# Optimization experiments

Measured on AMD Instinct MI355X. Metric: run time of the kernel, lower is better.

Reference implementation:

```python
import jax, jax.numpy as jnp
import numpy as np

H = 12  # num_attention_heads


def setup_inputs() -> dict:
    key = jax.random.key(0)
    ks = jax.random.split(key, 7)
    B, T, L, D = 4, 64, 128, 768
    input_ids = jax.random.randint(ks[0], (B, T, L), 0, 30000, dtype=jnp.int32)
    speaker_ids = jax.random.randint(ks[1], (B, T), 0, 8, dtype=jnp.int32)
    token_embeddings = jax.random.normal(ks[2], (B, T, L, D), dtype=jnp.float32)
    edu_embeddings = jax.random.normal(ks[3], (B, T, D), dtype=jnp.float32)
    s = 1.0 / np.sqrt(D)
    Wk = jax.random.normal(ks[4], (D, D), dtype=jnp.float32) * s
    Wv = jax.random.normal(ks[5], (D, D), dtype=jnp.float32) * s
    Wq = jax.random.normal(ks[6], (D, D), dtype=jnp.float32) * s
    return {"input_ids": input_ids, "speaker_ids": speaker_ids,
            "token_embeddings": token_embeddings, "edu_embeddings": edu_embeddings,
            "Wk": Wk, "Wv": Wv, "Wq": Wq}


def reference(input_ids, speaker_ids, token_embeddings, edu_embeddings, Wk, Wv, Wq):
    B, T, L = input_ids.shape
    D = token_embeddings.shape[-1]
    d = D // H
    # per-turn keys/values, split into heads: [B,T,H,d]
    k = (edu_embeddings @ Wk.T).reshape(B, T, H, d)
    v = (edu_embeddings @ Wv.T).reshape(B, T, H, d)
    # per-head outer products k (x) v: [B,T,H,d,d]
    kv = jnp.einsum('bthd,bthe->bthde', k, v)
    # speaker-segmented inclusive prefix sum: M[b,t] = sum_{u<=t, spk[u]==spk[t]} kv[b,u]
    same = speaker_ids[:, None, :] == speaker_ids[:, :, None]        # [B,T(t),T(u)]
    causal = jnp.tril(jnp.ones((T, T), dtype=bool))                  # u <= t (inclusive)
    A = (same & causal).astype(kv.dtype)                             # [B,T,T]
    M = jnp.einsum('btu,buhde->bthde', A, kv)                        # [B,T,H,d,d]
    # token queries attend into their turn's speaker memory matrix
    q = (token_embeddings @ Wq.T).reshape(B, T, L, H, d)
    a = jnp.einsum('btlhd,bthde->btlhe', q, M).reshape(B, T, L, D)
    return token_embeddings + a
```

## Files before the change

### kernel.cpp

```cpp
#include <hip/hip_runtime.h>
#include <hip/hip_bf16.h>

#define NB 4
#define NT 64
#define NL 128
#define ND 768
#define NH 12
#define HD 64

typedef __attribute__((ext_vector_type(8))) short short8;
typedef __attribute__((ext_vector_type(4))) float f32x4;

typedef __attribute__((address_space(3))) unsigned int lds_u32;
typedef __attribute__((address_space(1))) const unsigned int glob_u32;

static __device__ __forceinline__ unsigned short f2b(float x) {
    __hip_bfloat16 h = __float2bfloat16(x);
    return *reinterpret_cast<unsigned short*>(&h);
}
static __device__ __forceinline__ float b2f(unsigned short u) {
    unsigned int v = ((unsigned int)u) << 16;
    union { unsigned int i; float f; } c; c.i = v; return c.f;
}
static __device__ __forceinline__ void gl2lds16(const void* g, void* l) {
    __builtin_amdgcn_global_load_lds((glob_u32*)g, (lds_u32*)l, 16, 0, 0);
}

#define TE_C   3145728u
#define WQ_C   3219456u
#define EDU_C  3244032u
#define WK_C   3317760u
#define NCHUNK 3391488u

__global__ __launch_bounds__(256) void conv_bf16(
    const float* __restrict__ te, const float* __restrict__ Wq,
    const float* __restrict__ edu, const float* __restrict__ Wk,
    const float* __restrict__ Wv, unsigned short* __restrict__ dst)
{
    for (size_t c = (size_t)blockIdx.x * 256 + threadIdx.x; c < (size_t)NCHUNK;
         c += (size_t)2048 * 256) {
        const float* s;
        if (c < TE_C)       s = te  + c * 8;
        else if (c < WQ_C)  s = Wq  + (c - TE_C)  * 8;
        else if (c < EDU_C) s = edu + (c - WQ_C)  * 8;
        else if (c < WK_C)  s = Wk  + (c - EDU_C) * 8;
        else                s = Wv  + (c - WK_C)  * 8;
        float4 x = *(const float4*)s;
        float4 y = *(const float4*)(s + 4);
        unsigned short v[8];
        v[0] = f2b(x.x); v[1] = f2b(x.y); v[2] = f2b(x.z); v[3] = f2b(x.w);
        v[4] = f2b(y.x); v[5] = f2b(y.y); v[6] = f2b(y.z); v[7] = f2b(y.w);
        *(short8*)(dst + c * 8) = *(short8*)v;
    }
}

__global__ __launch_bounds__(256) void kvm(
    const unsigned short* __restrict__ edu_b,
    const unsigned short* __restrict__ wk_b,
    const unsigned short* __restrict__ wv_b,
    const int* __restrict__ spk,
    unsigned short* __restrict__ Mt)
{
    const int h = blockIdx.x, b = blockIdx.y, eh = blockIdx.z;

    __shared__ float bucket[8][32][65];
    __shared__ float k_s[64][68];
    __shared__ float v_s[64][36];
    __shared__ __align__(16) unsigned short stage[10240];
    __shared__ int spk_s[64];
    unsigned short* edu_s = stage;
    unsigned short* wk_s  = stage + 4096;
    unsigned short* wv_s  = stage + 8192;

    const int tid = threadIdx.x, lane = tid & 63, wvx = tid >> 6;
    const int lr = lane & 15, lg = lane >> 4, r8 = lane >> 3, l8 = lane & 7;

    { float* p = &bucket[0][0][0];
      for (int i = tid; i < 8 * 32 * 65; i += 256) p[i] = 0.f; }
    if (tid < 64) spk_s[tid] = spk[b * NT + tid];

    const unsigned short* edub = edu_b + (size_t)(b * 64) * ND;
    const unsigned short* wkb  = wk_b + (size_t)(h * 64) * ND;
    const unsigned short* wvb  = wv_b + (size_t)(h * 64 + eh * 32) * ND;

    f32x4 acc_k[4], acc_v[2];
    #pragma unroll
    for (int i = 0; i < 4; i++) acc_k[i] = (f32x4){0.f, 0.f, 0.f, 0.f};
    #pragma unroll
    for (int i = 0; i < 2; i++) acc_v[i] = (f32x4){0.f, 0.f, 0.f, 0.f};

    const int sswz = ((l8 ^ r8) * 8);

    for (int k0 = 0; k0 < ND; k0 += 64) {
        __syncthreads();
        #pragma unroll
        for (int j = 0; j < 5; j++) {
            const int cid = wvx * 5 + j;
            const unsigned short* gs; unsigned short* ls;
            if (cid < 8)       { gs = edub + (size_t)(cid * 8 + r8) * ND;        ls = edu_s + cid * 512; }
            else if (cid < 16) { gs = wkb  + (size_t)((cid - 8) * 8 + r8) * ND;  ls = wk_s + (cid - 8) * 512; }
            else               { gs = wvb  + (size_t)((cid - 16) * 8 + r8) * ND; ls = wv_s + (cid - 16) * 512; }
            gl2lds16(gs + k0 + sswz, ls);
        }
        __syncthreads();
        #pragma unroll
        for (int k32 = 0; k32 < 2; k32++) {
            const int cx = (((k32 * 4 + lg) ^ (lr & 7)) * 8);
            short8 eb = *(const short8*)&edu_s[(wvx * 16 + lr) * 64 + cx];
            #pragma unroll
            for (int jb = 0; jb < 4; jb++) {
                short8 ak = *(const short8*)&wk_s[(jb * 16 + lr) * 64 + cx];
                acc_k[jb] = __builtin_amdgcn_mfma_f32_16x16x32_bf16(ak, eb, acc_k[jb], 0, 0, 0);
            }
            #pragma unroll
            for (int jb = 0; jb < 2; jb++) {
                short8 av = *(const short8*)&wv_s[(jb * 16 + lr) * 64 + cx];
                acc_v[jb] = __builtin_amdgcn_mfma_f32_16x16x32_bf16(av, eb, acc_v[jb], 0, 0, 0);
            }
        }
    }

    {
        const int t = wvx * 16 + lr;
        #pragma unroll
        for (int jb = 0; jb < 4; jb++) *(f32x4*)&k_s[t][jb * 16 + lg * 4] = acc_k[jb];
        #pragma unroll
        for (int jb = 0; jb < 2; jb++) *(f32x4*)&v_s[t][jb * 16 + lg * 4] = acc_v[jb];
    }
    __syncthreads();

    const int e = tid & 31, dg = tid >> 5;
    for (int t = 0; t < NT; t++) {
        const int s = spk_s[t];
        const float vv = v_s[t][e];
        unsigned short tmp[8];
        #pragma unroll
        for (int jj = 0; jj < 8; jj++) {
            float m = bucket[s][e][dg * 8 + jj] + k_s[t][dg * 8 + jj] * vv;
            bucket[s][e][dg * 8 + jj] = m;
            tmp[jj] = f2b(m);
        }
        unsigned short* mpp = Mt + (((size_t)(b * NT + t) * NH + h) * HD + eh * 32 + e) * HD + dg * 8;
        *(short8*)mpp = *(short8*)tmp;
    }
}

__global__ __launch_bounds__(256, 2) void fused_qm(
    const unsigned short* __restrict__ te_b,
    const unsigned short* __restrict__ wq_b,
    const unsigned short* __restrict__ Mt,
    float* __restrict__ out)
{
    const int orig = blockIdx.x;
    const int id   = (orig & 7) * 192 + (orig >> 3);
    const int hp   = id % 6;
    const int bt   = id / 6;

    __shared__ __align__(16) unsigned short smem[40960];
    unsigned short* mt_s = smem + 32768;
    unsigned short* q_s  = smem;

    const int tid  = threadIdx.x;
    const int lane = tid & 63;
    const int wvx  = tid >> 6;
    const int lr   = lane & 15;
    const int lg   = lane >> 4;
    const int wm   = wvx >> 1;
    const int wn   = wvx & 1;
    const int r8   = lane >> 3;
    const int l8   = lane & 7;
    const int sswz = (l8 ^ r8) * 8;

    const unsigned short* teb = te_b + (size_t)bt * NL * ND;
    const unsigned short* wqb = wq_b + (size_t)hp * 128 * ND;

    {
        const unsigned short* mp = Mt + ((size_t)bt * NH + hp * 2) * (HD * HD);
        #pragma unroll
        for (int j = 0; j < 4; j++) {
            const int off = wvx * 2048 + j * 512;
            gl2lds16(mp + off + r8 * 64 + sswz, mt_s + off);
        }
    }

    f32x4 acc[4][4];
    #pragma unroll
    for (int i = 0; i < 4; i++)
        #pragma unroll
        for (int j = 0; j < 4; j++) acc[i][j] = (f32x4){0.f, 0.f, 0.f, 0.f};

    auto STAGE = [&](int bb, int k0) {
        #pragma unroll
        for (int j = 0; j < 4; j++) {
            const int rbase = wvx * 32 + j * 8;
            gl2lds16(teb + (size_t)(rbase + r8) * ND + k0 + sswz,
                     smem + bb + rbase * 64);
            gl2lds16(wqb + (size_t)(rbase + r8) * ND + k0 + sswz,
                     smem + bb + 8192 + rbase * 64);
        }
    };
    auto COMPUTE = [&](int bb) {
        const unsigned short* tes = smem + bb;
        const unsigned short* wqs = smem + bb + 8192;
        #pragma unroll
        for (int k32 = 0; k32 < 2; k32++) {
            const int cx = (((k32 * 4 + lg) ^ (lr & 7)) * 8);
            short8 af[4], bf[4];
            #pragma unroll
            for (int tm = 0; tm < 4; tm++)
                af[tm] = *(const short8*)&wqs[(wm * 64 + tm * 16 + lr) * 64 + cx];
            #pragma unroll
            for (int tn = 0; tn < 4; tn++)
                bf[tn] = *(const short8*)&tes[(wn * 64 + tn * 16 + lr) * 64 + cx];
            #pragma unroll
            for (int tm = 0; tm < 4; tm++)
                #pragma unroll
                for (int tn = 0; tn < 4; tn++)
                    acc[tm][tn] = __builtin_amdgcn_mfma_f32_16x16x32_bf16(
                        af[tm], bf[tn], acc[tm][tn], 0, 0, 0);
        }
    };

    STAGE(0, 0);
    __syncthreads();
    for (int k0 = 0; k0 < ND; k0 += 128) {
        STAGE(16384, k0 + 64);
        COMPUTE(0);
        __syncthreads();
        if (k0 + 128 < ND) STAGE(0, k0 + 128);
        COMPUTE(16384);
        __syncthreads();
    }

    #pragma unroll
    for (int tm = 0; tm < 4; tm++) {
        const int d0 = wm * 64 + tm * 16 + lg * 4;
        #pragma unroll
        for (int tn = 0; tn < 4; tn++) {
            const int ltok = wn * 64 + tn * 16 + lr;
            f32x4 a = acc[tm][tn];
            uint2 w2;
            w2.x = (unsigned)f2b(a.x) | ((unsigned)f2b(a.y) << 16);
            w2.y = (unsigned)f2b(a.z) | ((unsigned)f2b(a.w) << 16);
            *(uint2*)&q_s[ltok * 136 + d0] = w2;
        }
    }
    __syncthreads();

    const int h2 = wvx & 1;
    const int lh = wvx >> 1;
    f32x4 acc2[4][4];
    #pragma unroll
    for (int i = 0; i < 4; i++)
        #pragma unroll
        for (int j = 0; j < 4; j++) acc2[i][j] = (f32x4){0.f, 0.f, 0.f, 0.f};

    #pragma unroll
    for (int k32 = 0; k32 < 2; k32++) {
        const int ko = k32 * 32 + lg * 8;
        const int cx = (((k32 * 4 + lg) ^ (lr & 7)) * 8);
        short8 af[4], bf[4];
        #pragma unroll
        for (int tm = 0; tm < 4; tm++)
            af[tm] = *(const short8*)&q_s[(lh * 64 + tm * 16 + lr) * 136 + h2 * 64 + ko];
        #pragma unroll
        for (int tn = 0; tn < 4; tn++)
            bf[tn] = *(const short8*)&mt_s[(h2 * 64 + tn * 16 + lr) * 64 + cx];
        #pragma unroll
        for (int tm = 0; tm < 4; tm++)
            #pragma unroll
            for (int tn = 0; tn < 4; tn++)
                acc2[tm][tn] = __builtin_amdgcn_mfma_f32_16x16x32_bf16(
                    af[tm], bf[tn], acc2[tm][tn], 0, 0, 0);
    }

    float* ob = out + (size_t)bt * NL * ND;
    #pragma unroll
    for (int tm = 0; tm < 4; tm++) {
        const int l0 = lh * 64 + tm * 16 + lg * 4;
        #pragma unroll
        for (int tn = 0; tn < 4; tn++) {
            const int cg = hp * 128 + h2 * 64 + tn * 16 + lr;
            f32x4 a = acc2[tm][tn];
            #pragma unroll
            for (int r = 0; r < 4; r++) {
                size_t gi = (size_t)(l0 + r) * ND + cg;
                ob[gi] = b2f(teb[gi]) + a[r];
            }
        }
    }
}

extern "C" void kernel_launch(void* const* d_in, const int* in_sizes, int n_in,
                              void* d_out, int out_size, void* d_ws, size_t ws_size,
                              hipStream_t stream)
{
    const int*   spk = (const int*)d_in[1];
    const float* te  = (const float*)d_in[2];
    const float* edu = (const float*)d_in[3];
    const float* Wk  = (const float*)d_in[4];
    const float* Wv  = (const float*)d_in[5];
    const float* Wq  = (const float*)d_in[6];
    float* out = (float*)d_out;

    unsigned short* bf    = (unsigned short*)d_ws;
    unsigned short* te_bb = bf;
    unsigned short* wq_bb = bf + 25165824u;
    unsigned short* edu_b = bf + 25755648u;
    unsigned short* wk_bb = bf + 25952256u;
    unsigned short* wv_bb = bf + 26542080u;
    unsigned short* Mtbuf = bf + 27131904u;

    conv_bf16<<<2048,            256, 0, stream>>>(te, Wq, edu, Wk, Wv, bf);
    kvm      <<<dim3(NH, NB, 2), 256, 0, stream>>>(edu_b, wk_bb, wv_bb, spk, Mtbuf);
    fused_qm <<<6 * NT * NB,     256, 0, stream>>>(te_bb, wq_bb, Mtbuf, out);
}
```

Baseline: 115.5 us.

## Unroll bf16 conversion, tighten GEMM pipeline waits, load M directly to registers

The conversion kernel now uses a fixed grid where each thread handles four chunks, with a dedicated fast path for token embeddings and all loads issued before the conversions. In the fused Q·M kernel, the K-loop double buffer is rewritten with explicit vmcnt/lgkmcnt waits and raw s_barriers so the next tile's loads stay in flight during compute. The M tile is read straight from global memory into registers instead of being staged through LDS, which shrinks shared memory from 80KB to 64KB. The hand-tuned waitcnt values and the unswizzled global reads of M risk correctness and uncoalesced access.

Result: no change. 114.4 us (-1.0%).

```diff
diff --git a/kernel.cpp b/kernel.cpp
--- a/kernel.cpp
+++ b/kernel.cpp
@@ -37,20 +37,34 @@
     const float* __restrict__ edu, const float* __restrict__ Wk,
     const float* __restrict__ Wv, unsigned short* __restrict__ dst)
 {
-    for (size_t c = (size_t)blockIdx.x * 256 + threadIdx.x; c < (size_t)NCHUNK;
-         c += (size_t)2048 * 256) {
-        const float* s;
-        if (c < TE_C)       s = te  + c * 8;
-        else if (c < WQ_C)  s = Wq  + (c - TE_C)  * 8;
-        else if (c < EDU_C) s = edu + (c - WQ_C)  * 8;
-        else if (c < WK_C)  s = Wk  + (c - EDU_C) * 8;
-        else                s = Wv  + (c - WK_C)  * 8;
-        float4 x = *(const float4*)s;
-        float4 y = *(const float4*)(s + 4);
+    const unsigned base = blockIdx.x * 1024u + threadIdx.x;
+    float4 x[4], y[4];
+    if (blockIdx.x < 3072u) {
+        #pragma unroll
+        for (int i = 0; i < 4; i++) {
+            const float* s = te + (size_t)(base + i * 256u) * 8u;
+            x[i] = *(const float4*)s;
+            y[i] = *(const float4*)(s + 4);
+        }
+    } else {
+        #pragma unroll
+        for (int i = 0; i < 4; i++) {
+            unsigned c = base + i * 256u;
+            const float* s;
+            if (c < WQ_C)       s = Wq  + (size_t)(c - TE_C)  * 8u;
+            else if (c < EDU_C) s = edu + (size_t)(c - WQ_C)  * 8u;
+            else if (c < WK_C)  s = Wk  + (size_t)(c - EDU_C) * 8u;
+            else                s = Wv  + (size_t)(c - WK_C)  * 8u;
+            x[i] = *(const float4*)s;
+            y[i] = *(const float4*)(s + 4);
+        }
+    }
+    #pragma unroll
+    for (int i = 0; i < 4; i++) {
         unsigned short v[8];
-        v[0] = f2b(x.x); v[1] = f2b(x.y); v[2] = f2b(x.z); v[3] = f2b(x.w);
-        v[4] = f2b(y.x); v[5] = f2b(y.y); v[6] = f2b(y.z); v[7] = f2b(y.w);
-        *(short8*)(dst + c * 8) = *(short8*)v;
+        v[0] = f2b(x[i].x); v[1] = f2b(x[i].y); v[2] = f2b(x[i].z); v[3] = f2b(x[i].w);
+        v[4] = f2b(y[i].x); v[5] = f2b(y[i].y); v[6] = f2b(y[i].z); v[7] = f2b(y[i].w);
+        *(short8*)(dst + (size_t)(base + i * 256u) * 8u) = *(short8*)v;
     }
 }
 
@@ -156,9 +170,12 @@
     const int hp   = id % 6;
     const int bt   = id / 6;
 
-    __shared__ __align__(16) unsigned short smem[40960];
-    unsigned short* mt_s = smem + 32768;
-    unsigned short* q_s  = smem;
+    __shared__ __align__(16) unsigned short smem[32768];
+    unsigned short* te0 = smem;
+    unsigned short* te1 = smem + 8192;
+    unsigned short* wq0 = smem + 16384;
+    unsigned short* wq1 = smem + 24576;
+    unsigned short* q_s = smem;
 
     const int tid  = threadIdx.x;
     const int lane = tid & 63;
@@ -174,62 +191,65 @@
     const unsigned short* teb = te_b + (size_t)bt * NL * ND;
     const unsigned short* wqb = wq_b + (size_t)hp * 128 * ND;
 
-    {
-        const unsigned short* mp = Mt + ((size_t)bt * NH + hp * 2) * (HD * HD);
-        #pragma unroll
-        for (int j = 0; j < 4; j++) {
-            const int off = wvx * 2048 + j * 512;
-            gl2lds16(mp + off + r8 * 64 + sswz, mt_s + off);
-        }
-    }
-
     f32x4 acc[4][4];
     #pragma unroll
     for (int i = 0; i < 4; i++)
         #pragma unroll
         for (int j = 0; j < 4; j++) acc[i][j] = (f32x4){0.f, 0.f, 0.f, 0.f};
 
-    auto STAGE = [&](int bb, int k0) {
+    auto STAGE = [&](unsigned short* tebuf, unsigned short* wqbuf, int k0) {
         #pragma unroll
         for (int j = 0; j < 4; j++) {
             const int rbase = wvx * 32 + j * 8;
-            gl2lds16(teb + (size_t)(rbase + r8) * ND + k0 + sswz,
-                     smem + bb + rbase * 64);
-            gl2lds16(wqb + (size_t)(rbase + r8) * ND + k0 + sswz,
-                     smem + bb + 8192 + rbase * 64);
+            gl2lds16(teb + (size_t)(rbase + r8) * ND + k0 + sswz, tebuf + rbase * 64);
+            gl2lds16(wqb + (size_t)(rbase + r8) * ND + k0 + sswz, wqbuf + rbase * 64);
         }
     };
-    auto COMPUTE = [&](int bb) {
-        const unsigned short* tes = smem + bb;
-        const unsigned short* wqs = smem + bb + 8192;
+    auto COMPUTE = [&](const unsigned short* tes, const unsigned short* wqs) {
         #pragma unroll
         for (int k32 = 0; k32 < 2; k32++) {
             const int cx = (((k32 * 4 + lg) ^ (lr & 7)) * 8);
-            short8 af[4], bf[4];
+            short8 af[4], bfv[4];
             #pragma unroll
             for (int tm = 0; tm < 4; tm++)
                 af[tm] = *(const short8*)&wqs[(wm * 64 + tm * 16 + lr) * 64 + cx];
             #pragma unroll
             for (int tn = 0; tn < 4; tn++)
-                bf[tn] = *(const short8*)&tes[(wn * 64 + tn * 16 + lr) * 64 + cx];
+                bfv[tn] = *(const short8*)&tes[(wn * 64 + tn * 16 + lr) * 64 + cx];
             #pragma unroll
             for (int tm = 0; tm < 4; tm++)
                 #pragma unroll
                 for (int tn = 0; tn < 4; tn++)
                     acc[tm][tn] = __builtin_amdgcn_mfma_f32_16x16x32_bf16(
-                        af[tm], bf[tn], acc[tm][tn], 0, 0, 0);
+                        af[tm], bfv[tn], acc[tm][tn], 0, 0, 0);
         }
     };
 
-    STAGE(0, 0);
-    __syncthreads();
-    for (int k0 = 0; k0 < ND; k0 += 128) {
-        STAGE(16384, k0 + 64);
-        COMPUTE(0);
-        __syncthreads();
-        if (k0 + 128 < ND) STAGE(0, k0 + 128);
-        COMPUTE(16384);
-        __syncthreads();
+    STAGE(te0, wq0, 0);
+    asm volatile("s_waitcnt vmcnt(0)" ::: "memory");
+    __builtin_amdgcn_sched_barrier(0);
+    __builtin_amdgcn_s_barrier();
+
+    #pragma unroll
+    for (int kt = 0; kt < 12; kt += 2) {
+        STAGE(te1, wq1, (kt + 1) * 64);
+        asm volatile("s_waitcnt vmcnt(8)" ::: "memory");
+        __builtin_amdgcn_sched_barrier(0);
+        __builtin_amdgcn_s_barrier();
+        COMPUTE(te0, wq0);
+        asm volatile("s_waitcnt lgkmcnt(0)" ::: "memory");
+        __builtin_amdgcn_s_barrier();
+        if (kt + 2 < 12) {
+            STAGE(te0, wq0, (kt + 2) * 64);
+            asm volatile("s_waitcnt vmcnt(8)" ::: "memory");
+        } else {
+            asm volatile("s_waitcnt vmcnt(0)" ::: "memory");
+        }
+        __builtin_amdgcn_sched_barrier(0);
+        __builtin_amdgcn_s_barrier();
+        COMPUTE(te1, wq1);
+        asm volatile("s_waitcnt lgkmcnt(0)" ::: "memory");
+        __builtin_amdgcn_s_barrier();
     }
 
     #pragma unroll
@@ -245,10 +265,19 @@
             *(uint2*)&q_s[ltok * 136 + d0] = w2;
         }
     }
-    __syncthreads();
 
     const int h2 = wvx & 1;
     const int lh = wvx >> 1;
+    const unsigned short* mp = Mt + ((size_t)(bt * NH) + hp * 2 + h2) * (HD * HD);
+    short8 bfr[8];
+    #pragma unroll
+    for (int tn = 0; tn < 4; tn++)
+        #pragma unroll
+        for (int k32 = 0; k32 < 2; k32++)
+            bfr[tn * 2 + k32] =
+                *(const short8*)&mp[(tn * 16 + lr) * 64 + k32 * 32 + lg * 8];
+    __syncthreads();
+
     f32x4 acc2[4][4];
     #pragma unroll
     for (int i = 0; i < 4; i++)
@@ -258,20 +287,16 @@
     #pragma unroll
     for (int k32 = 0; k32 < 2; k32++) {
         const int ko = k32 * 32 + lg * 8;
-        const int cx = (((k32 * 4 + lg) ^ (lr & 7)) * 8);
-        short8 af[4], bf[4];
+        short8 af[4];
         #pragma unroll
         for (int tm = 0; tm < 4; tm++)
             af[tm] = *(const short8*)&q_s[(lh * 64 + tm * 16 + lr) * 136 + h2 * 64 + ko];
         #pragma unroll
-        for (int tn = 0; tn < 4; tn++)
-            bf[tn] = *(const short8*)&mt_s[(h2 * 64 + tn * 16 + lr) * 64 + cx];
-        #pragma unroll
         for (int tm = 0; tm < 4; tm++)
             #pragma unroll
             for (int tn = 0; tn < 4; tn++)
                 acc2[tm][tn] = __builtin_amdgcn_mfma_f32_16x16x32_bf16(
-                    af[tm], bf[tn], acc2[tm][tn], 0, 0, 0);
+                    af[tm], bfr[tn * 2 + k32], acc2[tm][tn], 0, 0, 0);
     }
 
     float* ob = out + (size_t)bt * NL * ND;
@@ -311,7 +336,7 @@
     unsigned short* wv_bb = bf + 26542080u;
     unsigned short* Mtbuf = bf + 27131904u;
 
-    conv_bf16<<<2048,            256, 0, stream>>>(te, Wq, edu, Wk, Wv, bf);
+    conv_bf16<<<3312,            256, 0, stream>>>(te, Wq, edu, Wk, Wv, bf);
     kvm      <<<dim3(NH, NB, 2), 256, 0, stream>>>(edu_b, wk_bb, wv_bb, spk, Mtbuf);
     fused_qm <<<6 * NT * NB,     256, 0, stream>>>(te_bb, wq_bb, Mtbuf, out);
 }
```
